# Kernel optimization log

Measured on AMD Instinct MI355X. Metric: run time of the kernel, lower is better.

The kernel has to match this reference:

```python
import jax, jax.numpy as jnp
import numpy as np

B, H, W, C, G = 256, 64, 64, 3, 128
MH, INV = 10, 18
AS = MH + INV  # 28
EPS = 1e-5


def _bn(x, g, b):
    # training-mode BatchNorm2d: batch stats over (N,H,W), biased variance
    m = x.mean((0, 2, 3), keepdims=True)
    v = x.var((0, 2, 3), keepdims=True)
    return (x - m) * jax.lax.rsqrt(v + EPS) * g.reshape(1, -1, 1, 1) + b.reshape(1, -1, 1, 1)


def _ln(x, g, b):
    m = x.mean(-1, keepdims=True)
    v = x.var(-1, keepdims=True)
    return (x - m) * jax.lax.rsqrt(v + EPS) * g + b


def _conv(x, w, pad):
    return jax.lax.conv_general_dilated(x, w, (1, 1), [(pad, pad), (pad, pad)],
                                        dimension_numbers=('NCHW', 'OIHW', 'NCHW'))


def setup_inputs() -> dict:
    key = jax.random.key(0)
    ks = jax.random.split(key, 24)
    r = lambda i, shape, s=1.0: jax.random.normal(ks[i], shape, jnp.float32) * s
    return {
        'agent_state': r(0, (B, AS)),
        'world_state': r(1, (B, C, H, W)),
        'action': jax.random.uniform(ks[2], (B, 15), jnp.float32, 0.0, 2.999),
        # cnn params
        'bn1_g': jnp.ones((C,), jnp.float32), 'bn1_b': jnp.zeros((C,), jnp.float32),
        'conv1_w': r(3, (G, C, 1, 1), 0.5),
        'bn2_g': jnp.ones((G,), jnp.float32), 'bn2_b': jnp.zeros((G,), jnp.float32),
        'conv2_w': r(4, (G, G, 3, 3), 0.05),
        'bn3_g': jnp.ones((G,), jnp.float32), 'bn3_b': jnp.zeros((G,), jnp.float32),
        'fc1_w': r(5, (20, G), 0.1), 'fc1_b': r(6, (20,), 0.1),
        # mh_inventory
        'ln_mi_g': jnp.ones((AS,), jnp.float32), 'ln_mi_b': jnp.zeros((AS,), jnp.float32),
        'mi_w1': r(7, (100, AS), 0.2), 'mi_w2': r(8, (20, 100), 0.2),
        # action embeddings
        'emb_craft': r(9, (5, 3)), 'emb_equip': r(10, (8, 3)),
        'emb_ncraft': r(11, (8, 3)), 'emb_nsmelt': r(12, (3, 2)), 'emb_place': r(13, (7, 3)),
        # combined_actions
        'ln_ca_g': jnp.ones((24,), jnp.float32), 'ln_ca_b': jnp.zeros((24,), jnp.float32),
        'ca_w1': r(14, (100, 24), 0.2), 'ca_b1': r(15, (100,), 0.1),
        'ca_w2': r(16, (20, 100), 0.2), 'ca_b2': r(17, (20,), 0.1),
        # combined
        'ln_c_g': jnp.ones((60,), jnp.float32), 'ln_c_b': jnp.zeros((60,), jnp.float32),
        'c_w': r(18, (1, 60), 0.2),
        # dist_net
        'ln_d_g': jnp.ones((2 * AS,), jnp.float32), 'ln_d_b': jnp.zeros((2 * AS,), jnp.float32),
        'd_w1': r(19, (50, 2 * AS), 0.2), 'd_w2': r(20, (1, 50), 0.2),
    }


def reference(agent_state, world_state, action,
              bn1_g, bn1_b, conv1_w, bn2_g, bn2_b, conv2_w, bn3_g, bn3_b,
              fc1_w, fc1_b, ln_mi_g, ln_mi_b, mi_w1, mi_w2,
              emb_craft, emb_equip, emb_ncraft, emb_nsmelt, emb_place,
              ln_ca_g, ln_ca_b, ca_w1, ca_b1, ca_w2, ca_b2,
              ln_c_g, ln_c_b, c_w, ln_d_g, ln_d_b, d_w1, d_w2):
    relu = jax.nn.relu
    # ---- CNN branch ----
    x = relu(_bn(world_state, bn1_g, bn1_b))
    x = _conv(x, conv1_w, 0)                      # [B,G,H,W]
    x = relu(_bn(x, bn2_g, bn2_b))
    x = _conv(x, conv2_w, 1)                      # [B,G,H,W]
    x = x.mean((2, 3), keepdims=True)             # AvgPool2d((H,W)) -> [B,G,1,1]
    x = relu(_bn(x, bn3_g, bn3_b)).reshape(x.shape[0], -1)  # [B,G]
    x = relu(x @ fc1_w.T + fc1_b)                 # [B,20]
    # ---- agent-state MLP ----
    y = relu(relu(_ln(agent_state, ln_mi_g, ln_mi_b) @ mi_w1.T) @ mi_w2.T)  # [B,20]
    # ---- per-action embeddings / identities (ModuleDict order) ----
    ai = jax.lax.stop_gradient(action).astype(jnp.int32)
    parts = [action[:, 0:1], action[:, 1:2], action[:, 2:3], action[:, 3:4],
             emb_craft[ai[:, 4]], emb_equip[ai[:, 5]],
             action[:, 6:7], action[:, 7:8], action[:, 8:9],
             emb_ncraft[ai[:, 9]], emb_nsmelt[ai[:, 10]], emb_place[ai[:, 11]],
             action[:, 12:13], action[:, 13:14], action[:, 14:15]]
    acts = jnp.concatenate(parts, axis=1)         # [B,24]
    z = relu(relu(_ln(acts, ln_ca_g, ln_ca_b) @ ca_w1.T + ca_b1) @ ca_w2.T + ca_b2)  # [B,20]
    # ---- combined head ----
    c = jnp.tanh(_ln(jnp.concatenate([x, y, z], axis=1), ln_c_g, ln_c_b) @ c_w.T)    # [B,1]
    # ---- dist_net (previous_agent_state starts as zeros) ----
    prev = jnp.zeros_like(agent_state)
    sc = jnp.concatenate([prev, agent_state], axis=1)  # [B,2*AS]
    d = jnp.tanh(jnp.tanh(_ln(sc, ln_d_g, ln_d_b) @ d_w1.T) @ d_w2.T)                # [B,1]
    return (c, d)
```

## Files before the change

kernel.cpp:

```cpp
#include <hip/hip_runtime.h>
#include <math.h>

#define EPSF 1e-5f

constexpr int OFF_RED1 = 0;
constexpr int OFF_A1B1 = 384;
constexpr int OFF_RED2 = 512;
constexpr int OFF_W2E  = 4096;
constexpr int OFF_M    = OFF_W2E + 128 * 128 * 9;

__device__ __forceinline__ float wave_sum(float v) {
    #pragma unroll
    for (int off = 32; off > 0; off >>= 1) v += __shfl_down(v, off);
    return v;
}

__global__ __launch_bounds__(256) void kA(const float* __restrict__ x,
                                          const float* __restrict__ w2,
                                          float* __restrict__ red1,
                                          float* __restrict__ w2e) {
    int blk = blockIdx.x, tid = threadIdx.x;
    if (blk < 192) {
        int c = blk % 3, seg = blk / 3;
        float s = 0.f, s2 = 0.f;
        for (int bb = 0; bb < 4; ++bb) {
            int b = seg * 4 + bb;
            const float4* p = (const float4*)(x + (size_t)(b * 3 + c) * 4096);
            for (int i = tid; i < 1024; i += 256) {
                float4 v = p[i];
                s += v.x + v.y + v.z + v.w;
                s2 = fmaf(v.x, v.x, s2); s2 = fmaf(v.y, v.y, s2);
                s2 = fmaf(v.z, v.z, s2); s2 = fmaf(v.w, v.w, s2);
            }
        }
        __shared__ float ls[4], ls2[4];
        float ws_ = wave_sum(s), ws2_ = wave_sum(s2);
        if ((tid & 63) == 0) { ls[tid >> 6] = ws_; ls2[tid >> 6] = ws2_; }
        __syncthreads();
        if (tid == 0) {
            red1[blk * 2 + 0] = ls[0] + ls[1] + ls[2] + ls[3];
            red1[blk * 2 + 1] = ls2[0] + ls2[1] + ls2[2] + ls2[3];
        }
    } else {
        int idx = (blk - 192) * 256 + tid;
        int g = idx >> 7, gp = idx & 127;
        const float* wp = w2 + (size_t)(g * 128 + gp) * 9;
        float v0 = wp[0], v1 = wp[1], v2 = wp[2], v3 = wp[3], v4 = wp[4],
              v5 = wp[5], v6 = wp[6], v7 = wp[7], v8 = wp[8];
        float c[9];
        c[0] = ((v0 + v1) + (v2 + v3)) + ((v4 + v5) + (v6 + v7)) + v8;
        c[1] = -(v6 + v7 + v8);
        c[2] = -(v0 + v1 + v2);
        c[3] = -(v2 + v5 + v8);
        c[4] = -(v0 + v3 + v6);
        c[5] = v8; c[6] = v6; c[7] = v2; c[8] = v0;
        #pragma unroll
        for (int k = 0; k < 9; ++k) {
            int jj = gp * 9 + k;
            w2e[(size_t)(jj >> 2) * 512 + g * 4 + (jj & 3)] = c[k];
        }
    }
}

__global__ __launch_bounds__(256) void kB(const float* __restrict__ x,
                                          const float* __restrict__ red1,
                                          const float* __restrict__ g1,
                                          const float* __restrict__ b1,
                                          float* __restrict__ red2,
                                          float* __restrict__ a1b1) {
    __shared__ float ab[6];
    int b = blockIdx.x, tid = threadIdx.x;
    if (tid < 3) {
        float s = 0.f, s2 = 0.f;
        for (int seg = 0; seg < 64; ++seg) {
            s  += red1[(seg * 3 + tid) * 2 + 0];
            s2 += red1[(seg * 3 + tid) * 2 + 1];
        }
        float n = 256.f * 4096.f;
        float mean = s / n, var = s2 / n - mean * mean;
        float a = g1[tid] * rsqrtf(var + EPSF);
        ab[tid] = a; ab[3 + tid] = b1[tid] - mean * a;
        if (b == 0) { a1b1[tid] = a; a1b1[3 + tid] = ab[3 + tid]; }
    }
    __syncthreads();
    float A0 = ab[0], A1 = ab[1], A2 = ab[2];
    float B0 = ab[3], B1 = ab[4], B2 = ab[5];
    float acc[9] = {0, 0, 0, 0, 0, 0, 0, 0, 0};
    const float4* p0 = (const float4*)(x + (size_t)(b * 3 + 0) * 4096);
    const float4* p1 = (const float4*)(x + (size_t)(b * 3 + 1) * 4096);
    const float4* p2 = (const float4*)(x + (size_t)(b * 3 + 2) * 4096);
    for (int i = tid; i < 1024; i += 256) {
        float4 v0 = p0[i], v1 = p1[i], v2 = p2[i];
        #define MOM(e) { \
            float t0 = fmaxf(0.f, fmaf(A0, v0.e, B0)); \
            float t1 = fmaxf(0.f, fmaf(A1, v1.e, B1)); \
            float t2 = fmaxf(0.f, fmaf(A2, v2.e, B2)); \
            acc[0] += t0; acc[1] += t1; acc[2] += t2; \
            acc[3] = fmaf(t0, t0, acc[3]); acc[4] = fmaf(t0, t1, acc[4]); \
            acc[5] = fmaf(t0, t2, acc[5]); acc[6] = fmaf(t1, t1, acc[6]); \
            acc[7] = fmaf(t1, t2, acc[7]); acc[8] = fmaf(t2, t2, acc[8]); }
        MOM(x) MOM(y) MOM(z) MOM(w)
        #undef MOM
    }
    __shared__ float lw[4][9];
    #pragma unroll
    for (int k = 0; k < 9; ++k) {
        float v = wave_sum(acc[k]);
        if ((tid & 63) == 0) lw[tid >> 6][k] = v;
    }
    __syncthreads();
    if (tid == 0) {
        #pragma unroll
        for (int k = 0; k < 9; ++k)
            red2[b * 9 + k] = lw[0][k] + lw[1][k] + lw[2][k] + lw[3][k];
    }
}

__global__ __launch_bounds__(512) void kC(const float* __restrict__ x,
                                          const float* __restrict__ red2,
                                          const float* __restrict__ w1,
                                          const float* __restrict__ g2,
                                          const float* __restrict__ b2,
                                          const float* __restrict__ a1b1,
                                          const float* __restrict__ w2e,
                                          float* __restrict__ m) {
    __shared__ __align__(16) float lds[12288];
    __shared__ __align__(16) float Fsh[1152];
    __shared__ float wt[384], bt[128], momp[288], mom[9], ab[6];
    int b = blockIdx.x, tid = threadIdx.x;
    if (tid < 6) ab[tid] = a1b1[tid];
    if (tid < 288) {
        int seg = tid / 9, k = tid - seg * 9;
        float s = 0.f;
        #pragma unroll
        for (int r = 0; r < 8; ++r) s += red2[(seg * 8 + r) * 9 + k];
        momp[tid] = s;
    }
    __syncthreads();
    if (tid < 9) {
        float s = 0.f;
        #pragma unroll
        for (int sg = 0; sg < 32; ++sg) s += momp[sg * 9 + tid];
        mom[tid] = s / (256.f * 4096.f);
    }
    {
        float A0 = ab[0], A1 = ab[1], A2 = ab[2];
        float B0 = ab[3], B1 = ab[4], B2 = ab[5];
        const float4* xb = (const float4*)(x + (size_t)b * 3 * 4096);
        for (int i = tid; i < 3072; i += 512) {
            float4 v = xb[i];
            int c = i >> 10;
            float a = (c == 0) ? A0 : ((c == 1) ? A1 : A2);
            float bb = (c == 0) ? B0 : ((c == 1) ? B1 : B2);
            v.x = fmaxf(0.f, fmaf(a, v.x, bb));
            v.y = fmaxf(0.f, fmaf(a, v.y, bb));
            v.z = fmaxf(0.f, fmaf(a, v.z, bb));
            v.w = fmaxf(0.f, fmaf(a, v.w, bb));
            *(float4*)&lds[i << 2] = v;
        }
    }
    __syncthreads();
    if (tid < 128) {
        int g = tid;
        float wa = w1[g * 3 + 0], wb = w1[g * 3 + 1], wc = w1[g * 3 + 2];
        float mean = wa * mom[0] + wb * mom[1] + wc * mom[2];
        float ey2 = wa * wa * mom[3] + wb * wb * mom[6] + wc * wc * mom[8]
                  + 2.f * (wa * wb * mom[4] + wa * wc * mom[5] + wb * wc * mom[7]);
        float var = ey2 - mean * mean;
        float a = g2[g] * rsqrtf(var + EPSF);
        wt[g * 3 + 0] = a * wa; wt[g * 3 + 1] = a * wb; wt[g * 3 + 2] = a * wc;
        bt[g] = b2[g] - mean * a;
    }
    __syncthreads();
    int gl = tid & 31, q = tid >> 5;
    {
        float w0[4], w1v[4], w2v[4], bw[4], S[4] = {0, 0, 0, 0};
        #pragma unroll
        for (int j = 0; j < 4; ++j) {
            int g = gl + 32 * j;
            w0[j] = wt[g * 3 + 0]; w1v[j] = wt[g * 3 + 1];
            w2v[j] = wt[g * 3 + 2]; bw[j] = bt[g];
        }
        int base = q * 256;
        #pragma unroll 4
        for (int i = 0; i < 64; ++i) {
            int pp = base + i * 4;
            float4 t0 = *(const float4*)&lds[pp];
            float4 t1 = *(const float4*)&lds[4096 + pp];
            float4 t2 = *(const float4*)&lds[8192 + pp];
            #pragma unroll
            for (int j = 0; j < 4; ++j) {
                float u0 = fmaxf(0.f, fmaf(w0[j], t0.x, fmaf(w1v[j], t1.x, fmaf(w2v[j], t2.x, bw[j]))));
                float u1 = fmaxf(0.f, fmaf(w0[j], t0.y, fmaf(w1v[j], t1.y, fmaf(w2v[j], t2.y, bw[j]))));
                float u2 = fmaxf(0.f, fmaf(w0[j], t0.z, fmaf(w1v[j], t1.z, fmaf(w2v[j], t2.z, bw[j]))));
                float u3 = fmaxf(0.f, fmaf(w0[j], t0.w, fmaf(w1v[j], t1.w, fmaf(w2v[j], t2.w, bw[j]))));
                S[j] += (u0 + u1) + (u2 + u3);
            }
        }
        {
            int g = tid & 127, task = tid >> 7;
            float vw0 = wt[g * 3 + 0], vw1 = wt[g * 3 + 1], vw2 = wt[g * 3 + 2], vb = bt[g];
            float s = 0.f, first = 0.f, last = 0.f;
            int p0 = (task == 1) ? 63 * 64 : ((task == 3) ? 63 : 0);
            int stp = (task >= 2) ? 64 : 1;
            #pragma unroll 4
            for (int i = 0; i < 64; ++i) {
                int p = p0 + i * stp;
                float u = fmaxf(0.f, fmaf(vw0, lds[p], fmaf(vw1, lds[4096 + p], fmaf(vw2, lds[8192 + p], vb))));
                s += u;
                if (i == 0) first = u;
                if (i == 63) last = u;
            }
            Fsh[g * 9 + 1 + task] = s;
            if (task == 0) { Fsh[g * 9 + 5] = first; Fsh[g * 9 + 6] = last; }
            if (task == 1) { Fsh[g * 9 + 7] = first; Fsh[g * 9 + 8] = last; }
        }
        __syncthreads();
        #pragma unroll
        for (int j = 0; j < 4; ++j) lds[(gl + 32 * j) * 17 + q] = S[j];
    }
    __syncthreads();
    if (tid < 128) {
        float s = 0.f;
        #pragma unroll
        for (int qq = 0; qq < 16; ++qq) s += lds[tid * 17 + qq];
        Fsh[tid * 9 + 0] = s;
    }
    __syncthreads();
    {
        int chunk = tid >> 7, g = tid & 127;
        float acc = 0.f;
        #pragma unroll 4
        for (int t = 0; t < 72; ++t) {
            int jb = chunk * 72 + t;
            float4 wv = *(const float4*)&w2e[(size_t)jb * 512 + g * 4];
            float4 fv = *(const float4*)&Fsh[jb * 4];
            acc = fmaf(wv.x, fv.x, fmaf(wv.y, fv.y, fmaf(wv.z, fv.z, fmaf(wv.w, fv.w, acc))));
        }
        __syncthreads();
        lds[chunk * 128 + g] = acc;
    }
    __syncthreads();
    if (tid < 128)
        m[b * 128 + tid] = (lds[tid] + lds[128 + tid] + lds[256 + tid] + lds[384 + tid]) * (1.f / 4096.f);
}

__global__ __launch_bounds__(256) void kE(
    const float* __restrict__ m, const float* __restrict__ g3, const float* __restrict__ b3,
    const float* __restrict__ agent, const float* __restrict__ action,
    const float* __restrict__ fc1w, const float* __restrict__ fc1b,
    const float* __restrict__ lnmig, const float* __restrict__ lnmib,
    const float* __restrict__ miw1, const float* __restrict__ miw2,
    const float* __restrict__ embc, const float* __restrict__ embe,
    const float* __restrict__ embnc, const float* __restrict__ embns,
    const float* __restrict__ embp,
    const float* __restrict__ lncag, const float* __restrict__ lncab,
    const float* __restrict__ caw1, const float* __restrict__ cab1,
    const float* __restrict__ caw2, const float* __restrict__ cab2,
    const float* __restrict__ lncg, const float* __restrict__ lncb,
    const float* __restrict__ cw,
    const float* __restrict__ lndg, const float* __restrict__ lndb,
    const float* __restrict__ dw1, const float* __restrict__ dw2,
    float* __restrict__ out) {
    __shared__ float red[4][128];
    __shared__ float xsh[128];
    __shared__ float lnv[28], lnca[24], lnsc[56], h1[100], h2[100], h3[50], cat[60];
    int b = blockIdx.x, tid = threadIdx.x;
    {
        int g = tid & 127, half = tid >> 7;
        float s = 0.f, s2 = 0.f;
        for (int i = 0; i < 128; ++i) {
            float v = m[(half * 128 + i) * 128 + g];
            s += v; s2 = fmaf(v, v, s2);
        }
        red[half * 2 + 0][g] = s;
        red[half * 2 + 1][g] = s2;
    }
    __syncthreads();
    if (tid < 128) {
        float s = red[0][tid] + red[2][tid], s2 = red[1][tid] + red[3][tid];
        float mean = s / 256.f, var = s2 / 256.f - mean * mean;
        float a = g3[tid] * rsqrtf(var + EPSF);
        float bb = b3[tid] - mean * a;
        xsh[tid] = fmaxf(0.f, fmaf(a, m[b * 128 + tid], bb));
    }
    int l = tid & 63, w = tid >> 6;
    if (w == 0) {
        float av = (l < 28) ? agent[b * 28 + l] : 0.f;
        float s = wave_sum(av), s2 = wave_sum(av * av);
        s = __shfl(s, 0); s2 = __shfl(s2, 0);
        float mean = s / 28.f, var = s2 / 28.f - mean * mean;
        float rs = rsqrtf(var + EPSF);
        if (l < 28) lnv[l] = (av - mean) * rs * lnmig[l] + lnmib[l];
    } else if (w == 1) {
        const float* ab = action + b * 15;
        float actv = 0.f;
        if (l < 24) {
            if (l < 4)       actv = ab[l];
            else if (l < 7)  { int ix = (int)ab[4];  actv = embc[ix * 3 + (l - 4)]; }
            else if (l < 10) { int ix = (int)ab[5];  actv = embe[ix * 3 + (l - 7)]; }
            else if (l < 13) actv = ab[l - 4];
            else if (l < 16) { int ix = (int)ab[9];  actv = embnc[ix * 3 + (l - 13)]; }
            else if (l < 18) { int ix = (int)ab[10]; actv = embns[ix * 2 + (l - 16)]; }
            else if (l < 21) { int ix = (int)ab[11]; actv = embp[ix * 3 + (l - 18)]; }
            else             actv = ab[l - 9];
        }
        float s = wave_sum(actv), s2 = wave_sum(actv * actv);
        s = __shfl(s, 0); s2 = __shfl(s2, 0);
        float mean = s / 24.f, var = s2 / 24.f - mean * mean;
        float rs = rsqrtf(var + EPSF);
        if (l < 24) lnca[l] = (actv - mean) * rs * lncag[l] + lncab[l];
    } else if (w == 2) {
        float g1v = (l < 56) ? agent[b * 28 + (l < 28 ? l : l - 28)] : 0.f;
        float av = (l < 28) ? g1v : 0.f;
        float s = wave_sum(av), s2 = wave_sum(av * av);
        s = __shfl(s, 0); s2 = __shfl(s2, 0);
        float mean = s / 56.f, var = s2 / 56.f - mean * mean;
        float rs = rsqrtf(var + EPSF);
        if (l < 56) {
            float vv = (l < 28) ? 0.f : g1v;
            lnsc[l] = (vv - mean) * rs * lndg[l] + lndb[l];
        }
    }
    __syncthreads();
    if (tid < 100) {
        float a = 0.f;
        for (int i = 0; i < 28; ++i) a = fmaf(miw1[tid * 28 + i], lnv[i], a);
        h1[tid] = fmaxf(0.f, a);
    } else if (tid < 200) {
        int j = tid - 100;
        float a = cab1[j];
        for (int i = 0; i < 24; ++i) a = fmaf(caw1[j * 24 + i], lnca[i], a);
        h2[j] = fmaxf(0.f, a);
    } else if (tid < 250) {
        int j = tid - 200;
        float a = 0.f;
        for (int i = 0; i < 56; ++i) a = fmaf(dw1[j * 56 + i], lnsc[i], a);
        h3[j] = tanhf(a);
    }
    __syncthreads();
    if (tid < 20) {
        float a = 0.f;
        for (int i = 0; i < 100; ++i) a = fmaf(miw2[tid * 100 + i], h1[i], a);
        cat[20 + tid] = fmaxf(0.f, a);
    } else if (tid >= 64 && tid < 84) {
        int j = tid - 64;
        float a = cab2[j];
        for (int i = 0; i < 100; ++i) a = fmaf(caw2[j * 100 + i], h2[i], a);
        cat[40 + j] = fmaxf(0.f, a);
    } else if (tid >= 128 && tid < 148) {
        int j = tid - 128;
        float a = fc1b[j];
        for (int i = 0; i < 128; ++i) a = fmaf(fc1w[j * 128 + i], xsh[i], a);
        cat[j] = fmaxf(0.f, a);
    } else if (tid >= 192) {
        int l3 = tid - 192;
        float dt = (l3 < 50) ? dw2[l3] * h3[l3] : 0.f;
        dt = wave_sum(dt);
        if (l3 == 0) out[256 + b] = tanhf(dt);
    }
    __syncthreads();
    if (w == 0) {
        float cv = (l < 60) ? cat[l] : 0.f;
        float ss = wave_sum(cv), ss2 = wave_sum(cv * cv);
        ss = __shfl(ss, 0); ss2 = __shfl(ss2, 0);
        float mean60 = ss / 60.f, var60 = ss2 / 60.f - mean60 * mean60;
        float rs60 = rsqrtf(var60 + EPSF);
        float term = (l < 60) ? cw[l] * ((cv - mean60) * rs60 * lncg[l] + lncb[l]) : 0.f;
        term = wave_sum(term);
        if (l == 0) out[b] = tanhf(term);
    }
}

extern "C" void kernel_launch(void* const* d_in, const int* in_sizes, int n_in,
                              void* d_out, int out_size, void* d_ws, size_t ws_size,
                              hipStream_t stream) {
    (void)in_sizes; (void)n_in; (void)out_size; (void)ws_size;
    const float* agent  = (const float*)d_in[0];
    const float* world  = (const float*)d_in[1];
    const float* action = (const float*)d_in[2];
    const float* bn1_g  = (const float*)d_in[3];
    const float* bn1_b  = (const float*)d_in[4];
    const float* conv1w = (const float*)d_in[5];
    const float* bn2_g  = (const float*)d_in[6];
    const float* bn2_b  = (const float*)d_in[7];
    const float* conv2w = (const float*)d_in[8];
    const float* bn3_g  = (const float*)d_in[9];
    const float* bn3_b  = (const float*)d_in[10];
    const float* fc1w   = (const float*)d_in[11];
    const float* fc1b   = (const float*)d_in[12];
    const float* lnmig  = (const float*)d_in[13];
    const float* lnmib  = (const float*)d_in[14];
    const float* miw1   = (const float*)d_in[15];
    const float* miw2   = (const float*)d_in[16];
    const float* embc   = (const float*)d_in[17];
    const float* embe   = (const float*)d_in[18];
    const float* embnc  = (const float*)d_in[19];
    const float* embns  = (const float*)d_in[20];
    const float* embp   = (const float*)d_in[21];
    const float* lncag  = (const float*)d_in[22];
    const float* lncab  = (const float*)d_in[23];
    const float* caw1   = (const float*)d_in[24];
    const float* cab1   = (const float*)d_in[25];
    const float* caw2   = (const float*)d_in[26];
    const float* cab2   = (const float*)d_in[27];
    const float* lncg   = (const float*)d_in[28];
    const float* lncb   = (const float*)d_in[29];
    const float* cw     = (const float*)d_in[30];
    const float* lndg   = (const float*)d_in[31];
    const float* lndb   = (const float*)d_in[32];
    const float* dw1    = (const float*)d_in[33];
    const float* dw2    = (const float*)d_in[34];
    float* out = (float*)d_out;
    float* ws = (float*)d_ws;

    hipLaunchKernelGGL(kA, dim3(256), dim3(256), 0, stream,
                       world, conv2w, ws + OFF_RED1, ws + OFF_W2E);
    hipLaunchKernelGGL(kB, dim3(256), dim3(256), 0, stream,
                       world, ws + OFF_RED1, bn1_g, bn1_b, ws + OFF_RED2, ws + OFF_A1B1);
    hipLaunchKernelGGL(kC, dim3(256), dim3(512), 0, stream,
                       world, ws + OFF_RED2, conv1w, bn2_g, bn2_b, ws + OFF_A1B1,
                       ws + OFF_W2E, ws + OFF_M);
    hipLaunchKernelGGL(kE, dim3(256), dim3(256), 0, stream,
                       ws + OFF_M, bn3_g, bn3_b, agent, action, fc1w, fc1b,
                       lnmig, lnmib, miw1, miw2,
                       embc, embe, embnc, embns, embp,
                       lncag, lncab, caw1, cab1, caw2, cab2,
                       lncg, lncb, cw, lndg, lndb, dw1, dw2, out);
}
```

Before: 187.3 us.

## Fuse four kernels into one cooperative kernel with grid syncs and LDS-resident input

Replaces the four-kernel pipeline with a single cooperative-launch kernel of 256 blocks. Grid-wide syncs separate the BN1 statistics, conv1 moment, conv2 and head phases. Each block loads its image into LDS once and reuses it for the BN1 stats, the moment accumulation and the conv stages, instead of reading the input from global memory three times. This removes the kernel launch gaps and the repeated input reads, in exchange for grid-sync overhead and the need for all 256 blocks of 512 threads to be co-resident.

```diff
diff --git a/kernel.cpp b/kernel.cpp
--- a/kernel.cpp
+++ b/kernel.cpp
@@ -1,12 +1,14 @@
 #include <hip/hip_runtime.h>
+#include <hip/hip_cooperative_groups.h>
 #include <math.h>
 
+namespace cg = cooperative_groups;
+
 #define EPSF 1e-5f
 
 constexpr int OFF_RED1 = 0;
-constexpr int OFF_A1B1 = 384;
-constexpr int OFF_RED2 = 512;
-constexpr int OFF_W2E  = 4096;
+constexpr int OFF_RED2 = 2048;
+constexpr int OFF_W2E  = 8192;
 constexpr int OFF_M    = OFF_W2E + 128 * 128 * 9;
 
 __device__ __forceinline__ float wave_sum(float v) {
@@ -15,143 +17,106 @@
     return v;
 }
 
-__global__ __launch_bounds__(256) void kA(const float* __restrict__ x,
-                                          const float* __restrict__ w2,
-                                          float* __restrict__ red1,
-                                          float* __restrict__ w2e) {
-    int blk = blockIdx.x, tid = threadIdx.x;
-    if (blk < 192) {
-        int c = blk % 3, seg = blk / 3;
-        float s = 0.f, s2 = 0.f;
-        for (int bb = 0; bb < 4; ++bb) {
-            int b = seg * 4 + bb;
-            const float4* p = (const float4*)(x + (size_t)(b * 3 + c) * 4096);
-            for (int i = tid; i < 1024; i += 256) {
-                float4 v = p[i];
-                s += v.x + v.y + v.z + v.w;
-                s2 = fmaf(v.x, v.x, s2); s2 = fmaf(v.y, v.y, s2);
-                s2 = fmaf(v.z, v.z, s2); s2 = fmaf(v.w, v.w, s2);
-            }
-        }
-        __shared__ float ls[4], ls2[4];
-        float ws_ = wave_sum(s), ws2_ = wave_sum(s2);
-        if ((tid & 63) == 0) { ls[tid >> 6] = ws_; ls2[tid >> 6] = ws2_; }
-        __syncthreads();
-        if (tid == 0) {
-            red1[blk * 2 + 0] = ls[0] + ls[1] + ls[2] + ls[3];
-            red1[blk * 2 + 1] = ls2[0] + ls2[1] + ls2[2] + ls2[3];
-        }
-    } else {
-        int idx = (blk - 192) * 256 + tid;
-        int g = idx >> 7, gp = idx & 127;
-        const float* wp = w2 + (size_t)(g * 128 + gp) * 9;
-        float v0 = wp[0], v1 = wp[1], v2 = wp[2], v3 = wp[3], v4 = wp[4],
-              v5 = wp[5], v6 = wp[6], v7 = wp[7], v8 = wp[8];
-        float c[9];
-        c[0] = ((v0 + v1) + (v2 + v3)) + ((v4 + v5) + (v6 + v7)) + v8;
-        c[1] = -(v6 + v7 + v8);
-        c[2] = -(v0 + v1 + v2);
-        c[3] = -(v2 + v5 + v8);
-        c[4] = -(v0 + v3 + v6);
-        c[5] = v8; c[6] = v6; c[7] = v2; c[8] = v0;
-        #pragma unroll
-        for (int k = 0; k < 9; ++k) {
-            int jj = gp * 9 + k;
-            w2e[(size_t)(jj >> 2) * 512 + g * 4 + (jj & 3)] = c[k];
-        }
-    }
-}
-
-__global__ __launch_bounds__(256) void kB(const float* __restrict__ x,
-                                          const float* __restrict__ red1,
-                                          const float* __restrict__ g1,
-                                          const float* __restrict__ b1,
-                                          float* __restrict__ red2,
-                                          float* __restrict__ a1b1) {
-    __shared__ float ab[6];
-    int b = blockIdx.x, tid = threadIdx.x;
-    if (tid < 3) {
-        float s = 0.f, s2 = 0.f;
-        for (int seg = 0; seg < 64; ++seg) {
-            s  += red1[(seg * 3 + tid) * 2 + 0];
-            s2 += red1[(seg * 3 + tid) * 2 + 1];
-        }
-        float n = 256.f * 4096.f;
-        float mean = s / n, var = s2 / n - mean * mean;
-        float a = g1[tid] * rsqrtf(var + EPSF);
-        ab[tid] = a; ab[3 + tid] = b1[tid] - mean * a;
-        if (b == 0) { a1b1[tid] = a; a1b1[3 + tid] = ab[3 + tid]; }
-    }
-    __syncthreads();
-    float A0 = ab[0], A1 = ab[1], A2 = ab[2];
-    float B0 = ab[3], B1 = ab[4], B2 = ab[5];
-    float acc[9] = {0, 0, 0, 0, 0, 0, 0, 0, 0};
-    const float4* p0 = (const float4*)(x + (size_t)(b * 3 + 0) * 4096);
-    const float4* p1 = (const float4*)(x + (size_t)(b * 3 + 1) * 4096);
-    const float4* p2 = (const float4*)(x + (size_t)(b * 3 + 2) * 4096);
-    for (int i = tid; i < 1024; i += 256) {
-        float4 v0 = p0[i], v1 = p1[i], v2 = p2[i];
-        #define MOM(e) { \
-            float t0 = fmaxf(0.f, fmaf(A0, v0.e, B0)); \
-            float t1 = fmaxf(0.f, fmaf(A1, v1.e, B1)); \
-            float t2 = fmaxf(0.f, fmaf(A2, v2.e, B2)); \
-            acc[0] += t0; acc[1] += t1; acc[2] += t2; \
-            acc[3] = fmaf(t0, t0, acc[3]); acc[4] = fmaf(t0, t1, acc[4]); \
-            acc[5] = fmaf(t0, t2, acc[5]); acc[6] = fmaf(t1, t1, acc[6]); \
-            acc[7] = fmaf(t1, t2, acc[7]); acc[8] = fmaf(t2, t2, acc[8]); }
-        MOM(x) MOM(y) MOM(z) MOM(w)
-        #undef MOM
-    }
-    __shared__ float lw[4][9];
-    #pragma unroll
-    for (int k = 0; k < 9; ++k) {
-        float v = wave_sum(acc[k]);
-        if ((tid & 63) == 0) lw[tid >> 6][k] = v;
-    }
-    __syncthreads();
-    if (tid == 0) {
-        #pragma unroll
-        for (int k = 0; k < 9; ++k)
-            red2[b * 9 + k] = lw[0][k] + lw[1][k] + lw[2][k] + lw[3][k];
-    }
-}
-
-__global__ __launch_bounds__(512) void kC(const float* __restrict__ x,
-                                          const float* __restrict__ red2,
-                                          const float* __restrict__ w1,
-                                          const float* __restrict__ g2,
-                                          const float* __restrict__ b2,
-                                          const float* __restrict__ a1b1,
-                                          const float* __restrict__ w2e,
-                                          float* __restrict__ m) {
+struct Prm {
+    const float *world, *agent, *action;
+    const float *bn1_g, *bn1_b, *conv1w, *bn2_g, *bn2_b, *conv2w, *bn3_g, *bn3_b;
+    const float *fc1w, *fc1b, *lnmig, *lnmib, *miw1, *miw2;
+    const float *embc, *embe, *embnc, *embns, *embp;
+    const float *lncag, *lncab, *caw1, *cab1, *caw2, *cab2, *lncg, *lncb, *cw;
+    const float *lndg, *lndb, *dw1, *dw2;
+    float *red1, *red2, *w2e, *m, *out;
+};
+
+__global__ __launch_bounds__(512) void kAll(Prm p) {
+    cg::grid_group grid = cg::this_grid();
     __shared__ __align__(16) float lds[12288];
     __shared__ __align__(16) float Fsh[1152];
     __shared__ float wt[384], bt[128], momp[288], mom[9], ab[6];
+    __shared__ float rw[8][10];
+    __shared__ float pp[96];
+    __shared__ float r8[8][128], xsh[128];
+    __shared__ float lnv[28], lnca[24], lnsc[56], h1[100], h2[100], h3[50], cat[60];
+
     int b = blockIdx.x, tid = threadIdx.x;
-    if (tid < 6) ab[tid] = a1b1[tid];
-    if (tid < 288) {
-        int seg = tid / 9, k = tid - seg * 9;
-        float s = 0.f;
-        #pragma unroll
-        for (int r = 0; r < 8; ++r) s += red2[(seg * 8 + r) * 9 + k];
-        momp[tid] = s;
-    }
-    __syncthreads();
-    if (tid < 9) {
-        float s = 0.f;
-        #pragma unroll
-        for (int sg = 0; sg < 32; ++sg) s += momp[sg * 9 + tid];
-        mom[tid] = s / (256.f * 4096.f);
-    }
+    int wv = tid >> 6, ln = tid & 63;
+
+    {
+        const float4* xb = (const float4*)(p.world + (size_t)b * 12288);
+        float s0 = 0, s1 = 0, s2 = 0, q0 = 0, q1 = 0, q2 = 0;
+        #pragma unroll
+        for (int k = 0; k < 6; ++k) {
+            int i = k * 512 + tid;
+            float4 v = xb[i];
+            *(float4*)&lds[i << 2] = v;
+            float t = (v.x + v.y) + (v.z + v.w);
+            float t2 = fmaf(v.x, v.x, fmaf(v.y, v.y, fmaf(v.z, v.z, v.w * v.w)));
+            if (k < 2)      { s0 += t; q0 += t2; }
+            else if (k < 4) { s1 += t; q1 += t2; }
+            else            { s2 += t; q2 += t2; }
+        }
+        float r0 = wave_sum(s0), r1 = wave_sum(s1), r2 = wave_sum(s2);
+        float r3 = wave_sum(q0), r4 = wave_sum(q1), r5 = wave_sum(q2);
+        if (ln == 0) {
+            rw[wv][0] = r0; rw[wv][1] = r1; rw[wv][2] = r2;
+            rw[wv][3] = r3; rw[wv][4] = r4; rw[wv][5] = r5;
+        }
+        __syncthreads();
+        if (tid < 6) {
+            float s = 0;
+            #pragma unroll
+            for (int w = 0; w < 8; ++w) s += rw[w][tid];
+            p.red1[b * 6 + tid] = s;
+        }
+        if (tid < 64) {
+            int idx = b * 64 + tid;
+            int g = idx >> 7, gp = idx & 127;
+            const float* wp = p.conv2w + (size_t)(g * 128 + gp) * 9;
+            float v0 = wp[0], v1 = wp[1], v2 = wp[2], v3 = wp[3], v4 = wp[4],
+                  v5 = wp[5], v6 = wp[6], v7 = wp[7], v8 = wp[8];
+            float c[9];
+            c[0] = ((v0 + v1) + (v2 + v3)) + ((v4 + v5) + (v6 + v7)) + v8;
+            c[1] = -(v6 + v7 + v8);
+            c[2] = -(v0 + v1 + v2);
+            c[3] = -(v2 + v5 + v8);
+            c[4] = -(v0 + v3 + v6);
+            c[5] = v8; c[6] = v6; c[7] = v2; c[8] = v0;
+            #pragma unroll
+            for (int k = 0; k < 9; ++k) {
+                int jj = gp * 9 + k;
+                p.w2e[(size_t)(jj >> 2) * 512 + g * 4 + (jj & 3)] = c[k];
+            }
+        }
+    }
+    __threadfence();
+    grid.sync();
+
+    if (tid < 96) {
+        int k = tid % 6, seg = tid / 6;
+        float s = 0;
+        #pragma unroll
+        for (int i = 0; i < 16; ++i) s += p.red1[(seg * 16 + i) * 6 + k];
+        pp[seg * 6 + k] = s;
+    }
+    __syncthreads();
+    if (tid < 3) {
+        float s = 0, s2 = 0;
+        #pragma unroll
+        for (int seg = 0; seg < 16; ++seg) { s += pp[seg * 6 + tid]; s2 += pp[seg * 6 + 3 + tid]; }
+        float n = 256.f * 4096.f;
+        float mean = s / n, var = s2 / n - mean * mean;
+        float a = p.bn1_g[tid] * rsqrtf(var + EPSF);
+        ab[tid] = a; ab[3 + tid] = p.bn1_b[tid] - mean * a;
+    }
+    __syncthreads();
     {
         float A0 = ab[0], A1 = ab[1], A2 = ab[2];
         float B0 = ab[3], B1 = ab[4], B2 = ab[5];
-        const float4* xb = (const float4*)(x + (size_t)b * 3 * 4096);
-        for (int i = tid; i < 3072; i += 512) {
-            float4 v = xb[i];
-            int c = i >> 10;
-            float a = (c == 0) ? A0 : ((c == 1) ? A1 : A2);
-            float bb = (c == 0) ? B0 : ((c == 1) ? B1 : B2);
+        #pragma unroll
+        for (int k = 0; k < 6; ++k) {
+            int i = k * 512 + tid;
+            float4 v = *(float4*)&lds[i << 2];
+            float a = (k < 2) ? A0 : ((k < 4) ? A1 : A2);
+            float bb = (k < 2) ? B0 : ((k < 4) ? B1 : B2);
             v.x = fmaxf(0.f, fmaf(a, v.x, bb));
             v.y = fmaxf(0.f, fmaf(a, v.y, bb));
             v.z = fmaxf(0.f, fmaf(a, v.z, bb));
@@ -160,20 +125,60 @@
         }
     }
     __syncthreads();
+    {
+        float acc[9] = {0, 0, 0, 0, 0, 0, 0, 0, 0};
+        for (int ii = tid; ii < 4096; ii += 512) {
+            float t0 = lds[ii], t1 = lds[4096 + ii], t2 = lds[8192 + ii];
+            acc[0] += t0; acc[1] += t1; acc[2] += t2;
+            acc[3] = fmaf(t0, t0, acc[3]); acc[4] = fmaf(t0, t1, acc[4]);
+            acc[5] = fmaf(t0, t2, acc[5]); acc[6] = fmaf(t1, t1, acc[6]);
+            acc[7] = fmaf(t1, t2, acc[7]); acc[8] = fmaf(t2, t2, acc[8]);
+        }
+        #pragma unroll
+        for (int k = 0; k < 9; ++k) {
+            float v = wave_sum(acc[k]);
+            if (ln == 0) rw[wv][k] = v;
+        }
+        __syncthreads();
+        if (tid < 9) {
+            float s = 0;
+            #pragma unroll
+            for (int w = 0; w < 8; ++w) s += rw[w][tid];
+            p.red2[b * 9 + tid] = s;
+        }
+    }
+    __threadfence();
+    grid.sync();
+
+    if (tid < 288) {
+        int seg = tid / 9, k = tid - seg * 9;
+        float s = 0.f;
+        #pragma unroll
+        for (int r = 0; r < 8; ++r) s += p.red2[(seg * 8 + r) * 9 + k];
+        momp[tid] = s;
+    }
+    __syncthreads();
+    if (tid < 9) {
+        float s = 0.f;
+        #pragma unroll
+        for (int sg = 0; sg < 32; ++sg) s += momp[sg * 9 + tid];
+        mom[tid] = s / (256.f * 4096.f);
+    }
+    __syncthreads();
     if (tid < 128) {
         int g = tid;
-        float wa = w1[g * 3 + 0], wb = w1[g * 3 + 1], wc = w1[g * 3 + 2];
+        float wa = p.conv1w[g * 3 + 0], wb = p.conv1w[g * 3 + 1], wc = p.conv1w[g * 3 + 2];
         float mean = wa * mom[0] + wb * mom[1] + wc * mom[2];
         float ey2 = wa * wa * mom[3] + wb * wb * mom[6] + wc * wc * mom[8]
                   + 2.f * (wa * wb * mom[4] + wa * wc * mom[5] + wb * wc * mom[7]);
         float var = ey2 - mean * mean;
-        float a = g2[g] * rsqrtf(var + EPSF);
+        float a = p.bn2_g[g] * rsqrtf(var + EPSF);
         wt[g * 3 + 0] = a * wa; wt[g * 3 + 1] = a * wb; wt[g * 3 + 2] = a * wc;
-        bt[g] = b2[g] - mean * a;
-    }
-    __syncthreads();
-    int gl = tid & 31, q = tid >> 5;
-    {
+        bt[g] = p.bn2_b[g] - mean * a;
+    }
+    __syncthreads();
+    {
+        int gl = tid & 31, q = tid >> 5;
         float w0[4], w1v[4], w2v[4], bw[4], S[4] = {0, 0, 0, 0};
         #pragma unroll
         for (int j = 0; j < 4; ++j) {
@@ -184,10 +189,10 @@
         int base = q * 256;
         #pragma unroll 4
         for (int i = 0; i < 64; ++i) {
-            int pp = base + i * 4;
-            float4 t0 = *(const float4*)&lds[pp];
-            float4 t1 = *(const float4*)&lds[4096 + pp];
-            float4 t2 = *(const float4*)&lds[8192 + pp];
+            int ppx = base + i * 4;
+            float4 t0 = *(const float4*)&lds[ppx];
+            float4 t1 = *(const float4*)&lds[4096 + ppx];
+            float4 t2 = *(const float4*)&lds[8192 + ppx];
             #pragma unroll
             for (int j = 0; j < 4; ++j) {
                 float u0 = fmaxf(0.f, fmaf(w0[j], t0.x, fmaf(w1v[j], t1.x, fmaf(w2v[j], t2.x, bw[j]))));
@@ -205,8 +210,8 @@
             int stp = (task >= 2) ? 64 : 1;
             #pragma unroll 4
             for (int i = 0; i < 64; ++i) {
-                int p = p0 + i * stp;
-                float u = fmaxf(0.f, fmaf(vw0, lds[p], fmaf(vw1, lds[4096 + p], fmaf(vw2, lds[8192 + p], vb))));
+                int px = p0 + i * stp;
+                float u = fmaxf(0.f, fmaf(vw0, lds[px], fmaf(vw1, lds[4096 + px], fmaf(vw2, lds[8192 + px], vb))));
                 s += u;
                 if (i == 0) first = u;
                 if (i == 63) last = u;
@@ -233,85 +238,65 @@
         #pragma unroll 4
         for (int t = 0; t < 72; ++t) {
             int jb = chunk * 72 + t;
-            float4 wv = *(const float4*)&w2e[(size_t)jb * 512 + g * 4];
+            float4 wvv = *(const float4*)&p.w2e[(size_t)jb * 512 + g * 4];
             float4 fv = *(const float4*)&Fsh[jb * 4];
-            acc = fmaf(wv.x, fv.x, fmaf(wv.y, fv.y, fmaf(wv.z, fv.z, fmaf(wv.w, fv.w, acc))));
+            acc = fmaf(wvv.x, fv.x, fmaf(wvv.y, fv.y, fmaf(wvv.z, fv.z, fmaf(wvv.w, fv.w, acc))));
         }
         __syncthreads();
         lds[chunk * 128 + g] = acc;
     }
     __syncthreads();
     if (tid < 128)
-        m[b * 128 + tid] = (lds[tid] + lds[128 + tid] + lds[256 + tid] + lds[384 + tid]) * (1.f / 4096.f);
-}
-
-__global__ __launch_bounds__(256) void kE(
-    const float* __restrict__ m, const float* __restrict__ g3, const float* __restrict__ b3,
-    const float* __restrict__ agent, const float* __restrict__ action,
-    const float* __restrict__ fc1w, const float* __restrict__ fc1b,
-    const float* __restrict__ lnmig, const float* __restrict__ lnmib,
-    const float* __restrict__ miw1, const float* __restrict__ miw2,
-    const float* __restrict__ embc, const float* __restrict__ embe,
-    const float* __restrict__ embnc, const float* __restrict__ embns,
-    const float* __restrict__ embp,
-    const float* __restrict__ lncag, const float* __restrict__ lncab,
-    const float* __restrict__ caw1, const float* __restrict__ cab1,
-    const float* __restrict__ caw2, const float* __restrict__ cab2,
-    const float* __restrict__ lncg, const float* __restrict__ lncb,
-    const float* __restrict__ cw,
-    const float* __restrict__ lndg, const float* __restrict__ lndb,
-    const float* __restrict__ dw1, const float* __restrict__ dw2,
-    float* __restrict__ out) {
-    __shared__ float red[4][128];
-    __shared__ float xsh[128];
-    __shared__ float lnv[28], lnca[24], lnsc[56], h1[100], h2[100], h3[50], cat[60];
-    int b = blockIdx.x, tid = threadIdx.x;
-    {
-        int g = tid & 127, half = tid >> 7;
+        p.m[b * 128 + tid] = (lds[tid] + lds[128 + tid] + lds[256 + tid] + lds[384 + tid]) * (1.f / 4096.f);
+    __threadfence();
+    grid.sync();
+
+    {
+        int g = tid & 127, quarter = tid >> 7;
         float s = 0.f, s2 = 0.f;
-        for (int i = 0; i < 128; ++i) {
-            float v = m[(half * 128 + i) * 128 + g];
+        for (int i = 0; i < 64; ++i) {
+            float v = p.m[(quarter * 64 + i) * 128 + g];
             s += v; s2 = fmaf(v, v, s2);
         }
-        red[half * 2 + 0][g] = s;
-        red[half * 2 + 1][g] = s2;
+        r8[quarter][g] = s; r8[4 + quarter][g] = s2;
     }
     __syncthreads();
     if (tid < 128) {
-        float s = red[0][tid] + red[2][tid], s2 = red[1][tid] + red[3][tid];
+        float s = r8[0][tid] + r8[1][tid] + r8[2][tid] + r8[3][tid];
+        float s2 = r8[4][tid] + r8[5][tid] + r8[6][tid] + r8[7][tid];
         float mean = s / 256.f, var = s2 / 256.f - mean * mean;
-        float a = g3[tid] * rsqrtf(var + EPSF);
-        float bb = b3[tid] - mean * a;
-        xsh[tid] = fmaxf(0.f, fmaf(a, m[b * 128 + tid], bb));
-    }
-    int l = tid & 63, w = tid >> 6;
+        float a = p.bn3_g[tid] * rsqrtf(var + EPSF);
+        float bb = p.bn3_b[tid] - mean * a;
+        xsh[tid] = fmaxf(0.f, fmaf(a, p.m[b * 128 + tid], bb));
+    }
+    int l = ln, w = wv;
     if (w == 0) {
-        float av = (l < 28) ? agent[b * 28 + l] : 0.f;
+        float av = (l < 28) ? p.agent[b * 28 + l] : 0.f;
         float s = wave_sum(av), s2 = wave_sum(av * av);
         s = __shfl(s, 0); s2 = __shfl(s2, 0);
         float mean = s / 28.f, var = s2 / 28.f - mean * mean;
         float rs = rsqrtf(var + EPSF);
-        if (l < 28) lnv[l] = (av - mean) * rs * lnmig[l] + lnmib[l];
+        if (l < 28) lnv[l] = (av - mean) * rs * p.lnmig[l] + p.lnmib[l];
     } else if (w == 1) {
-        const float* ab = action + b * 15;
+        const float* abp = p.action + b * 15;
         float actv = 0.f;
         if (l < 24) {
-            if (l < 4)       actv = ab[l];
-            else if (l < 7)  { int ix = (int)ab[4];  actv = embc[ix * 3 + (l - 4)]; }
-            else if (l < 10) { int ix = (int)ab[5];  actv = embe[ix * 3 + (l - 7)]; }
-            else if (l < 13) actv = ab[l - 4];
-            else if (l < 16) { int ix = (int)ab[9];  actv = embnc[ix * 3 + (l - 13)]; }
-            else if (l < 18) { int ix = (int)ab[10]; actv = embns[ix * 2 + (l - 16)]; }
-            else if (l < 21) { int ix = (int)ab[11]; actv = embp[ix * 3 + (l - 18)]; }
-            else             actv = ab[l - 9];
+            if (l < 4)       actv = abp[l];
+            else if (l < 7)  { int ix = (int)abp[4];  actv = p.embc[ix * 3 + (l - 4)]; }
+            else if (l < 10) { int ix = (int)abp[5];  actv = p.embe[ix * 3 + (l - 7)]; }
+            else if (l < 13) actv = abp[l - 4];
+            else if (l < 16) { int ix = (int)abp[9];  actv = p.embnc[ix * 3 + (l - 13)]; }
+            else if (l < 18) { int ix = (int)abp[10]; actv = p.embns[ix * 2 + (l - 16)]; }
+            else if (l < 21) { int ix = (int)abp[11]; actv = p.embp[ix * 3 + (l - 18)]; }
+            else             actv = abp[l - 9];
         }
         float s = wave_sum(actv), s2 = wave_sum(actv * actv);
         s = __shfl(s, 0); s2 = __shfl(s2, 0);
         float mean = s / 24.f, var = s2 / 24.f - mean * mean;
         float rs = rsqrtf(var + EPSF);
-        if (l < 24) lnca[l] = (actv - mean) * rs * lncag[l] + lncab[l];
+        if (l < 24) lnca[l] = (actv - mean) * rs * p.lncag[l] + p.lncab[l];
     } else if (w == 2) {
-        float g1v = (l < 56) ? agent[b * 28 + (l < 28 ? l : l - 28)] : 0.f;
+        float g1v = (l < 56) ? p.agent[b * 28 + (l < 28 ? l : l - 28)] : 0.f;
         float av = (l < 28) ? g1v : 0.f;
         float s = wave_sum(av), s2 = wave_sum(av * av);
         s = __shfl(s, 0); s2 = __shfl(s2, 0);
@@ -319,45 +304,45 @@
         float rs = rsqrtf(var + EPSF);
         if (l < 56) {
             float vv = (l < 28) ? 0.f : g1v;
-            lnsc[l] = (vv - mean) * rs * lndg[l] + lndb[l];
+            lnsc[l] = (vv - mean) * rs * p.lndg[l] + p.lndb[l];
         }
     }
     __syncthreads();
     if (tid < 100) {
         float a = 0.f;
-        for (int i = 0; i < 28; ++i) a = fmaf(miw1[tid * 28 + i], lnv[i], a);
+        for (int i = 0; i < 28; ++i) a = fmaf(p.miw1[tid * 28 + i], lnv[i], a);
         h1[tid] = fmaxf(0.f, a);
     } else if (tid < 200) {
         int j = tid - 100;
-        float a = cab1[j];
-        for (int i = 0; i < 24; ++i) a = fmaf(caw1[j * 24 + i], lnca[i], a);
+        float a = p.cab1[j];
+        for (int i = 0; i < 24; ++i) a = fmaf(p.caw1[j * 24 + i], lnca[i], a);
         h2[j] = fmaxf(0.f, a);
     } else if (tid < 250) {
         int j = tid - 200;
         float a = 0.f;
-        for (int i = 0; i < 56; ++i) a = fmaf(dw1[j * 56 + i], lnsc[i], a);
+        for (int i = 0; i < 56; ++i) a = fmaf(p.dw1[j * 56 + i], lnsc[i], a);
         h3[j] = tanhf(a);
     }
     __syncthreads();
     if (tid < 20) {
         float a = 0.f;
-        for (int i = 0; i < 100; ++i) a = fmaf(miw2[tid * 100 + i], h1[i], a);
+        for (int i = 0; i < 100; ++i) a = fmaf(p.miw2[tid * 100 + i], h1[i], a);
         cat[20 + tid] = fmaxf(0.f, a);
     } else if (tid >= 64 && tid < 84) {
         int j = tid - 64;
-        float a = cab2[j];
-        for (int i = 0; i < 100; ++i) a = fmaf(caw2[j * 100 + i], h2[i], a);
+        float a = p.cab2[j];
+        for (int i = 0; i < 100; ++i) a = fmaf(p.caw2[j * 100 + i], h2[i], a);
         cat[40 + j] = fmaxf(0.f, a);
     } else if (tid >= 128 && tid < 148) {
         int j = tid - 128;
-        float a = fc1b[j];
-        for (int i = 0; i < 128; ++i) a = fmaf(fc1w[j * 128 + i], xsh[i], a);
+        float a = p.fc1b[j];
+        for (int i = 0; i < 128; ++i) a = fmaf(p.fc1w[j * 128 + i], xsh[i], a);
         cat[j] = fmaxf(0.f, a);
-    } else if (tid >= 192) {
+    } else if (tid >= 192 && tid < 256) {
         int l3 = tid - 192;
-        float dt = (l3 < 50) ? dw2[l3] * h3[l3] : 0.f;
+        float dt = (l3 < 50) ? p.dw2[l3] * h3[l3] : 0.f;
         dt = wave_sum(dt);
-        if (l3 == 0) out[256 + b] = tanhf(dt);
+        if (l3 == 0) p.out[256 + b] = tanhf(dt);
     }
     __syncthreads();
     if (w == 0) {
@@ -366,9 +351,9 @@
         ss = __shfl(ss, 0); ss2 = __shfl(ss2, 0);
         float mean60 = ss / 60.f, var60 = ss2 / 60.f - mean60 * mean60;
         float rs60 = rsqrtf(var60 + EPSF);
-        float term = (l < 60) ? cw[l] * ((cv - mean60) * rs60 * lncg[l] + lncb[l]) : 0.f;
+        float term = (l < 60) ? p.cw[l] * ((cv - mean60) * rs60 * p.lncg[l] + p.lncb[l]) : 0.f;
         term = wave_sum(term);
-        if (l == 0) out[b] = tanhf(term);
+        if (l == 0) p.out[b] = tanhf(term);
     }
 }
 
@@ -376,55 +361,49 @@
                               void* d_out, int out_size, void* d_ws, size_t ws_size,
                               hipStream_t stream) {
     (void)in_sizes; (void)n_in; (void)out_size; (void)ws_size;
-    const float* agent  = (const float*)d_in[0];
-    const float* world  = (const float*)d_in[1];
-    const float* action = (const float*)d_in[2];
-    const float* bn1_g  = (const float*)d_in[3];
-    const float* bn1_b  = (const float*)d_in[4];
-    const float* conv1w = (const float*)d_in[5];
-    const float* bn2_g  = (const float*)d_in[6];
-    const float* bn2_b  = (const float*)d_in[7];
-    const float* conv2w = (const float*)d_in[8];
-    const float* bn3_g  = (const float*)d_in[9];
-    const float* bn3_b  = (const float*)d_in[10];
-    const float* fc1w   = (const float*)d_in[11];
-    const float* fc1b   = (const float*)d_in[12];
-    const float* lnmig  = (const float*)d_in[13];
-    const float* lnmib  = (const float*)d_in[14];
-    const float* miw1   = (const float*)d_in[15];
-    const float* miw2   = (const float*)d_in[16];
-    const float* embc   = (const float*)d_in[17];
-    const float* embe   = (const float*)d_in[18];
-    const float* embnc  = (const float*)d_in[19];
-    const float* embns  = (const float*)d_in[20];
-    const float* embp   = (const float*)d_in[21];
-    const float* lncag  = (const float*)d_in[22];
-    const float* lncab  = (const float*)d_in[23];
-    const float* caw1   = (const float*)d_in[24];
-    const float* cab1   = (const float*)d_in[25];
-    const float* caw2   = (const float*)d_in[26];
-    const float* cab2   = (const float*)d_in[27];
-    const float* lncg   = (const float*)d_in[28];
-    const float* lncb   = (const float*)d_in[29];
-    const float* cw     = (const float*)d_in[30];
-    const float* lndg   = (const float*)d_in[31];
-    const float* lndb   = (const float*)d_in[32];
-    const float* dw1    = (const float*)d_in[33];
-    const float* dw2    = (const float*)d_in[34];
-    float* out = (float*)d_out;
     float* ws = (float*)d_ws;
-
-    hipLaunchKernelGGL(kA, dim3(256), dim3(256), 0, stream,
-                       world, conv2w, ws + OFF_RED1, ws + OFF_W2E);
-    hipLaunchKernelGGL(kB, dim3(256), dim3(256), 0, stream,
-                       world, ws + OFF_RED1, bn1_g, bn1_b, ws + OFF_RED2, ws + OFF_A1B1);
-    hipLaunchKernelGGL(kC, dim3(256), dim3(512), 0, stream,
-                       world, ws + OFF_RED2, conv1w, bn2_g, bn2_b, ws + OFF_A1B1,
-                       ws + OFF_W2E, ws + OFF_M);
-    hipLaunchKernelGGL(kE, dim3(256), dim3(256), 0, stream,
-                       ws + OFF_M, bn3_g, bn3_b, agent, action, fc1w, fc1b,
-                       lnmig, lnmib, miw1, miw2,
-                       embc, embe, embnc, embns, embp,
-                       lncag, lncab, caw1, cab1, caw2, cab2,
-                       lncg, lncb, cw, lndg, lndb, dw1, dw2, out);
+    Prm p;
+    p.agent  = (const float*)d_in[0];
+    p.world  = (const float*)d_in[1];
+    p.action = (const float*)d_in[2];
+    p.bn1_g  = (const float*)d_in[3];
+    p.bn1_b  = (const float*)d_in[4];
+    p.conv1w = (const float*)d_in[5];
+    p.bn2_g  = (const float*)d_in[6];
+    p.bn2_b  = (const float*)d_in[7];
+    p.conv2w = (const float*)d_in[8];
+    p.bn3_g  = (const float*)d_in[9];
+    p.bn3_b  = (const float*)d_in[10];
+    p.fc1w   = (const float*)d_in[11];
+    p.fc1b   = (const float*)d_in[12];
+    p.lnmig  = (const float*)d_in[13];
+    p.lnmib  = (const float*)d_in[14];
+    p.miw1   = (const float*)d_in[15];
+    p.miw2   = (const float*)d_in[16];
+    p.embc   = (const float*)d_in[17];
+    p.embe   = (const float*)d_in[18];
+    p.embnc  = (const float*)d_in[19];
+    p.embns  = (const float*)d_in[20];
+    p.embp   = (const float*)d_in[21];
+    p.lncag  = (const float*)d_in[22];
+    p.lncab  = (const float*)d_in[23];
+    p.caw1   = (const float*)d_in[24];
+    p.cab1   = (const float*)d_in[25];
+    p.caw2   = (const float*)d_in[26];
+    p.cab2   = (const float*)d_in[27];
+    p.lncg   = (const float*)d_in[28];
+    p.lncb   = (const float*)d_in[29];
+    p.cw     = (const float*)d_in[30];
+    p.lndg   = (const float*)d_in[31];
+    p.lndb   = (const float*)d_in[32];
+    p.dw1    = (const float*)d_in[33];
+    p.dw2    = (const float*)d_in[34];
+    p.red1 = ws + OFF_RED1;
+    p.red2 = ws + OFF_RED2;
+    p.w2e  = ws + OFF_W2E;
+    p.m    = ws + OFF_M;
+    p.out  = (float*)d_out;
+
+    void* args[] = { &p };
+    hipLaunchCooperativeKernel((void*)kAll, dim3(256), dim3(512), args, 0, stream);
 }
```

New measurement: 427.8 us. 128% more time.
